# Kernel tuning notes

Measured on AMD Instinct MI355X. Metric: run time of the kernel, lower is better.

## Reference

```python
import jax, jax.numpy as jnp
import numpy as np
import math

S, B, D = 1024, 8, 1024
H = 16
DK = D // H
F = 4096
EPS = 1e-5


def _layernorm(x, g, b):
    m = jnp.mean(x, axis=-1, keepdims=True)
    v = jnp.mean(jnp.square(x - m), axis=-1, keepdims=True)
    return (x - m) * jax.lax.rsqrt(v + EPS) * g + b


def setup_inputs() -> dict:
    key = jax.random.key(0)
    ks = jax.random.split(key, 16)
    sc = 0.02
    inp = {
        "src": jax.random.normal(ks[0], (S, B, D), dtype=jnp.float32),
        "pos": jax.random.normal(ks[1], (S, B, D), dtype=jnp.float32),
        "Wq": jax.random.normal(ks[2], (D, D), dtype=jnp.float32) * sc,
        "bq": jnp.zeros((D,), dtype=jnp.float32),
        "Wk": jax.random.normal(ks[3], (D, D), dtype=jnp.float32) * sc,
        "bk": jnp.zeros((D,), dtype=jnp.float32),
        "Wv": jax.random.normal(ks[4], (D, D), dtype=jnp.float32) * sc,
        "bv": jnp.zeros((D,), dtype=jnp.float32),
        "Wo": jax.random.normal(ks[5], (D, D), dtype=jnp.float32) * sc,
        "bo": jnp.zeros((D,), dtype=jnp.float32),
        "W1": jax.random.normal(ks[6], (D, F), dtype=jnp.float32) * sc,
        "b1": jnp.zeros((F,), dtype=jnp.float32),
        "W2": jax.random.normal(ks[7], (F, D), dtype=jnp.float32) * sc,
        "b2": jnp.zeros((D,), dtype=jnp.float32),
        "g1": jnp.ones((D,), dtype=jnp.float32),
        "be1": jnp.zeros((D,), dtype=jnp.float32),
        "g2": jnp.ones((D,), dtype=jnp.float32),
        "be2": jnp.zeros((D,), dtype=jnp.float32),
    }
    return inp


def reference(src, pos, Wq, bq, Wk, bk, Wv, bv, Wo, bo, W1, b1, W2, b2, g1, be1, g2, be2):
    # post-norm encoder layer; dropout = identity (eval mode)
    qk_in = src + pos                      # q = k = src + pos, value = src
    # to batch-first [B, S, D]
    qb = jnp.transpose(qk_in, (1, 0, 2))
    vb = jnp.transpose(src, (1, 0, 2))

    def split_heads(x):                    # [B,S,D] -> [B,H,S,DK]
        return jnp.transpose(x.reshape(B, S, H, DK), (0, 2, 1, 3))

    q = split_heads(qb @ Wq + bq)
    k = split_heads(qb @ Wk + bk)
    v = split_heads(vb @ Wv + bv)

    scores = jnp.einsum('bhqd,bhkd->bhqk', q, k) / math.sqrt(DK)
    attn = jax.nn.softmax(scores, axis=-1)             # [B,H,S,S]
    ctx = jnp.einsum('bhqk,bhkd->bhqd', attn, v)       # [B,H,S,DK]
    ctx = jnp.transpose(ctx, (0, 2, 1, 3)).reshape(B, S, D)
    attn_out = ctx @ Wo + bo                           # [B,S,D]
    attn_out = jnp.transpose(attn_out, (1, 0, 2))      # back to [S,B,D]

    x = _layernorm(src + attn_out, g1, be1)
    ffn = jax.nn.relu(x @ W1 + b1) @ W2 + b2
    out = _layernorm(x + ffn, g2, be2)
    return out, attn
```

## Files before the change

### kernel.cpp

```cpp
#include <hip/hip_runtime.h>
#include <stdint.h>

#define S_ 1024
#define B_ 8
#define D_ 1024
#define H_ 16
#define DK_ 64
#define F_ 4096
#define EPS_ 1e-5f

typedef __bf16 bf16_t;
typedef __attribute__((ext_vector_type(8))) __bf16 bf16x8;
typedef __attribute__((ext_vector_type(4))) __bf16 bf16x4;
typedef __attribute__((ext_vector_type(4))) float f32x4;

#define GLD16(gp, lp) __builtin_amdgcn_global_load_lds( \
    (__attribute__((address_space(1))) void*)(void*)(gp), \
    (__attribute__((address_space(3))) void*)(lp), 16, 0, 0)

#define BAR() __builtin_amdgcn_s_barrier()
#define SB0() __builtin_amdgcn_sched_barrier(0)
#define LG0() do { asm volatile("s_waitcnt lgkmcnt(0)" ::: "memory"); SB0(); } while (0)
#define VM6() asm volatile("s_waitcnt vmcnt(6)" ::: "memory")

template<int MODE>
__global__ __launch_bounds__(512, 2)
void gemm8p(const bf16_t* __restrict__ A, const bf16_t* __restrict__ Bt,
            const float* __restrict__ bias, const float* __restrict__ bias2,
            void* __restrict__ out, void* __restrict__ out2,
            int K, int lda, int ldb, int ldc)
{
    __shared__ __align__(16) bf16_t AsL[2][256][64];
    __shared__ __align__(16) bf16_t BsL[2][256][64];

    const int nwg = gridDim.x * gridDim.y;
    int flat = blockIdx.y * gridDim.x + blockIdx.x;
    flat = (flat & 7) * (nwg >> 3) + (flat >> 3);
    const int bx = flat % gridDim.x, by = flat / gridDim.x;
    const int rowBase = by * 256, colBase = bx * 256;

    const int tid = threadIdx.x;
    const int lane = tid & 63;
    const int wave = tid >> 6;
    const int wr = wave >> 2, wc = wave & 3;
    const int lr = lane & 15, quad = lane >> 4;

    const int r0 = tid >> 3, r1 = 64 + r0;
    const int cs = (tid & 7) ^ (r0 & 7);
    const int cl = tid & 7;
    const bf16_t* a0p = A + (size_t)(rowBase + r0) * lda + cs * 8;
    const bf16_t* a1p = A + (size_t)(rowBase + r1) * lda + cs * 8;
    const bf16_t* b0p = Bt + (size_t)(colBase + r0) * ldb + cs * 8;
    const bf16_t* b1p = Bt + (size_t)(colBase + r1) * ldb + cs * 8;

#define STAGE_A(buf, h, kel) do { \
    GLD16(a0p + (size_t)(h) * 128 * lda + (kel), &AsL[buf][(h) * 128 + r0][cl * 8]); \
    GLD16(a1p + (size_t)(h) * 128 * lda + (kel), &AsL[buf][(h) * 128 + r1][cl * 8]); } while (0)
#define STAGE_B(buf, h, kel) do { \
    GLD16(b0p + (size_t)(h) * 128 * ldb + (kel), &BsL[buf][(h) * 128 + r0][cl * 8]); \
    GLD16(b1p + (size_t)(h) * 128 * ldb + (kel), &BsL[buf][(h) * 128 + r1][cl * 8]); } while (0)

#define RDA(buf, qm, AF) do { \
    _Pragma("unroll") for (int mi = 0; mi < 4; ++mi) { \
        const int r_ = (qm) * 128 + wr * 64 + mi * 16 + lr; \
        _Pragma("unroll") for (int kk = 0; kk < 2; ++kk) \
            AF[mi * 2 + kk] = *(const bf16x8*)&AsL[buf][r_][((kk * 4 + quad) ^ (lr & 7)) * 8]; } } while (0)
#define RDB(buf, qn, BF) do { \
    _Pragma("unroll") for (int ni = 0; ni < 2; ++ni) { \
        const int r_ = (qn) * 128 + wc * 32 + ni * 16 + lr; \
        _Pragma("unroll") for (int kk = 0; kk < 2; ++kk) \
            BF[ni * 2 + kk] = *(const bf16x8*)&BsL[buf][r_][((kk * 4 + quad) ^ (lr & 7)) * 8]; } } while (0)

#define MQ(qm, qn, AF, BF) do { \
    __builtin_amdgcn_s_setprio(1); \
    _Pragma("unroll") for (int kk = 0; kk < 2; ++kk) \
    _Pragma("unroll") for (int mi = 0; mi < 4; ++mi) \
    _Pragma("unroll") for (int ni = 0; ni < 2; ++ni) \
        acc[(qm) * 4 + mi][(qn) * 2 + ni] = __builtin_amdgcn_mfma_f32_16x16x32_bf16( \
            AF[mi * 2 + kk], BF[ni * 2 + kk], acc[(qm) * 4 + mi][(qn) * 2 + ni], 0, 0, 0); \
    __builtin_amdgcn_s_setprio(0); } while (0)

    f32x4 acc[8][4] = {};
    bf16x8 af[8], bq0[4], bq1[4];

    STAGE_A(0, 0, 0); STAGE_B(0, 0, 0); STAGE_B(0, 1, 0); STAGE_A(0, 1, 0);
    STAGE_A(1, 0, 64); STAGE_B(1, 0, 64); STAGE_B(1, 1, 64);
    VM6();
    BAR(); SB0();

    const int NT = K >> 6;
    const int kCap = K - 64;
    for (int it = 0; it < (NT >> 1); ++it) {
        const int kP1 = it * 128 + 64;
        int kN0 = it * 128 + 128; if (kN0 > kCap) kN0 = kCap;
        int kN1 = it * 128 + 192; if (kN1 > kCap) kN1 = kCap;

        RDA(0, 0, af); RDB(0, 0, bq0);
        STAGE_A(1, 1, kP1);
        BAR(); LG0();
        MQ(0, 0, af, bq0);
        BAR(); SB0();
        RDB(0, 1, bq1);
        STAGE_A(0, 0, kN0);
        BAR(); LG0();
        MQ(0, 1, af, bq1);
        BAR(); SB0();
        RDA(0, 1, af);
        STAGE_B(0, 0, kN0);
        BAR(); LG0();
        MQ(1, 1, af, bq1);
        BAR(); SB0();
        STAGE_B(0, 1, kN0);
        BAR(); SB0();
        MQ(1, 0, af, bq0);
        VM6();
        BAR(); SB0();
        RDA(1, 0, af); RDB(1, 0, bq0);
        STAGE_A(0, 1, kN0);
        BAR(); LG0();
        MQ(0, 0, af, bq0);
        BAR(); SB0();
        RDB(1, 1, bq1);
        STAGE_A(1, 0, kN1);
        BAR(); LG0();
        MQ(0, 1, af, bq1);
        BAR(); SB0();
        RDA(1, 1, af);
        STAGE_B(1, 0, kN1);
        BAR(); LG0();
        MQ(1, 1, af, bq1);
        BAR(); SB0();
        STAGE_B(1, 1, kN1);
        BAR(); SB0();
        MQ(1, 0, af, bq0);
        VM6();
        BAR(); SB0();
    }

#pragma unroll
    for (int mi = 0; mi < 8; ++mi) {
#pragma unroll
        for (int ni = 0; ni < 4; ++ni) {
            const int col = colBase + (ni >> 1) * 128 + wc * 32 + (ni & 1) * 16 + lr;
            float bv;
            if constexpr (MODE == 0) bv = (col < 1024) ? bias[col] : bias2[col - 1024];
            else bv = bias[col];
#pragma unroll
            for (int e = 0; e < 4; ++e) {
                const int row = rowBase + (mi >> 2) * 128 + wr * 64 + (mi & 3) * 16 + quad * 4 + e;
                const float v = acc[mi][ni][e] + bv;
                if constexpr (MODE == 0) {
                    const int sel = col >> 10, c10 = col & 1023;
                    const int s = row >> 3, b = row & 7, h = c10 >> 6, dk = c10 & 63;
                    bf16_t* dst = sel ? (bf16_t*)out2 : (bf16_t*)out;
                    dst[(((size_t)(b * 16 + h) * 1024 + s) << 6) + dk] = (bf16_t)v;
                } else {
                    ((bf16_t*)out)[(size_t)row * ldc + col] = (bf16_t)fmaxf(v, 0.f);
                }
            }
        }
    }
#undef STAGE_A
#undef STAGE_B
#undef RDA
#undef RDB
#undef MQ
}

template<int BM, int BN, int WM, int WN, int MODE>
__global__ __launch_bounds__(256)
void gemm_bt(const bf16_t* __restrict__ A, const bf16_t* __restrict__ Bt,
             const float* __restrict__ bias, void* __restrict__ out,
             int K, int lda, int ldb, int ldc, long batchA, long batchB)
{
    constexpr int MT = WM / 16, NT = WN / 16;
    constexpr int WCOLS = BN / WN;
    __shared__ __align__(16) bf16_t As[BM * 32];
    __shared__ __align__(16) bf16_t Bs[BN * 32];

    const int z = blockIdx.z;
    A += (size_t)z * batchA;
    Bt += (size_t)z * batchB;
    const int rowBase = blockIdx.y * BM;
    const int colBase = blockIdx.x * BN;
    const int tid = threadIdx.x;
    const int wave = tid >> 6, lane = tid & 63;
    const int wr = wave / WCOLS, wc = wave % WCOLS;
    const int lr = lane & 15;
    const int lk = (lane >> 4) * 8;

    f32x4 acc[MT][NT] = {};

    for (int k0 = 0; k0 < K; k0 += 32) {
#pragma unroll
        for (int i = 0; i < BM / 64; ++i) {
            int id = i * 256 + tid;
            GLD16(A + (size_t)(rowBase + (id >> 2)) * lda + k0 + (id & 3) * 8, As + id * 8);
        }
#pragma unroll
        for (int i = 0; i < BN / 64; ++i) {
            int id = i * 256 + tid;
            GLD16(Bt + (size_t)(colBase + (id >> 2)) * ldb + k0 + (id & 3) * 8, Bs + id * 8);
        }
        __syncthreads();
        bf16x8 af[MT], bfr[NT];
#pragma unroll
        for (int mi = 0; mi < MT; ++mi)
            af[mi] = *(const bf16x8*)&As[(wr * WM + mi * 16 + lr) * 32 + lk];
#pragma unroll
        for (int ni = 0; ni < NT; ++ni)
            bfr[ni] = *(const bf16x8*)&Bs[(wc * WN + ni * 16 + lr) * 32 + lk];
#pragma unroll
        for (int mi = 0; mi < MT; ++mi)
#pragma unroll
            for (int ni = 0; ni < NT; ++ni)
                acc[mi][ni] = __builtin_amdgcn_mfma_f32_16x16x32_bf16(af[mi], bfr[ni], acc[mi][ni], 0, 0, 0);
        __syncthreads();
    }

    const int quad = lane >> 4;
#pragma unroll
    for (int mi = 0; mi < MT; ++mi) {
#pragma unroll
        for (int ni = 0; ni < NT; ++ni) {
            const int col = colBase + wc * WN + ni * 16 + lr;
            float bv = bias[col];
#pragma unroll
            for (int e = 0; e < 4; ++e) {
                const int row = rowBase + wr * WM + mi * 16 + quad * 4 + e;
                float v = acc[mi][ni][e] + bv;
                if constexpr (MODE == 0) {
                    ((float*)out)[(size_t)row * ldc + col] = v;
                } else if constexpr (MODE == 2) {
                    int s = row >> 3, b = row & 7, h = col >> 6, dk = col & 63;
                    ((bf16_t*)out)[(((size_t)(b * 16 + h) * 64 + dk) << 10) + s] = (bf16_t)v;
                }
            }
        }
    }
}

__global__ __launch_bounds__(256)
void fused_attn(const bf16_t* __restrict__ qb, const bf16_t* __restrict__ kb,
                const bf16_t* __restrict__ vt, float* __restrict__ attn,
                bf16_t* __restrict__ ctx)
{
    __shared__ __align__(16) bf16_t Psh[32 * 1024];
    __shared__ float smax[4][32];
    __shared__ float ssum[4][32];

    int flat = blockIdx.y * 32 + blockIdx.x;
    flat = (flat & 7) * 512 + (flat >> 3);
    const int z = flat >> 5;
    const int qBase = (flat & 31) * 32;
    const int b = z >> 4, h = z & 15;
    const int tid = threadIdx.x;
    const int wave = tid >> 6, lane = tid & 63;
    const int lr = lane & 15, quad = lane >> 4;

    const bf16_t* Qz = qb + ((size_t)z << 16);
    const bf16_t* Kz = kb + ((size_t)z << 16);
    const bf16_t* Vz = vt + ((size_t)z << 16);
    float* Az = attn + ((size_t)z << 20);

    bf16x8 qf[2][2];
#pragma unroll
    for (int ni = 0; ni < 2; ++ni)
#pragma unroll
        for (int kk = 0; kk < 2; ++kk)
            qf[ni][kk] = *(const bf16x8*)(Qz + (size_t)(qBase + ni * 16 + lr) * 64 + kk * 32 + quad * 8);

    f32x4 acc[16][2] = {};
#pragma unroll
    for (int mi = 0; mi < 16; ++mi) {
        const bf16_t* kp = Kz + (size_t)(wave * 256 + mi * 16 + lr) * 64 + quad * 8;
        bf16x8 kf0 = *(const bf16x8*)kp;
        bf16x8 kf1 = *(const bf16x8*)(kp + 32);
#pragma unroll
        for (int ni = 0; ni < 2; ++ni) {
            acc[mi][ni] = __builtin_amdgcn_mfma_f32_16x16x32_bf16(kf0, qf[ni][0], acc[mi][ni], 0, 0, 0);
            acc[mi][ni] = __builtin_amdgcn_mfma_f32_16x16x32_bf16(kf1, qf[ni][1], acc[mi][ni], 0, 0, 0);
        }
    }

    float mloc[2];
#pragma unroll
    for (int ni = 0; ni < 2; ++ni) {
        float mx = acc[0][ni][0];
#pragma unroll
        for (int mi = 0; mi < 16; ++mi)
            mx = fmaxf(mx, fmaxf(fmaxf(acc[mi][ni][0], acc[mi][ni][1]),
                                 fmaxf(acc[mi][ni][2], acc[mi][ni][3])));
        mx = fmaxf(mx, __shfl_xor(mx, 16, 64));
        mx = fmaxf(mx, __shfl_xor(mx, 32, 64));
        mloc[ni] = mx;
    }
    if (quad == 0) { smax[wave][lr] = mloc[0]; smax[wave][16 + lr] = mloc[1]; }
    __syncthreads();

    float rs[2];
#pragma unroll
    for (int ni = 0; ni < 2; ++ni) {
        const int qh = ni * 16 + lr;
        const float mm = 0.125f * fmaxf(fmaxf(smax[0][qh], smax[1][qh]),
                                        fmaxf(smax[2][qh], smax[3][qh]));
        float s = 0.f;
#pragma unroll
        for (int mi = 0; mi < 16; ++mi)
#pragma unroll
            for (int e = 0; e < 4; ++e) {
                float p = __expf(fmaf(acc[mi][ni][e], 0.125f, -mm));
                acc[mi][ni][e] = p; s += p;
            }
        s += __shfl_xor(s, 16, 64);
        s += __shfl_xor(s, 32, 64);
        rs[ni] = s;
    }
    if (quad == 0) { ssum[wave][lr] = rs[0]; ssum[wave][16 + lr] = rs[1]; }
    __syncthreads();

#pragma unroll
    for (int ni = 0; ni < 2; ++ni) {
        const int qh = ni * 16 + lr;
        const float r = 1.0f / (ssum[0][qh] + ssum[1][qh] + ssum[2][qh] + ssum[3][qh]);
        float* arow = Az + ((size_t)(qBase + qh) << 10);
#pragma unroll
        for (int mi = 0; mi < 16; ++mi) {
            const int k0 = wave * 256 + mi * 16 + quad * 4;
            float4 o;
            o.x = acc[mi][ni][0] * r; o.y = acc[mi][ni][1] * r;
            o.z = acc[mi][ni][2] * r; o.w = acc[mi][ni][3] * r;
            *(float4*)(arow + k0) = o;
            bf16x4 pb;
            pb[0] = (bf16_t)o.x; pb[1] = (bf16_t)o.y; pb[2] = (bf16_t)o.z; pb[3] = (bf16_t)o.w;
            int byte = qh * 2048 + k0 * 2;
            byte ^= (qh & 7) << 4;
            *(bf16x4*)((char*)Psh + byte) = pb;
        }
    }
    __syncthreads();

    f32x4 cacc[2] = {};
#pragma unroll
    for (int kt = 0; kt < 32; ++kt) {
        bf16x8 vf = *(const bf16x8*)(Vz + (size_t)(wave * 16 + lr) * 1024 + kt * 32 + quad * 8);
#pragma unroll
        for (int mi = 0; mi < 2; ++mi) {
            const int qh = mi * 16 + lr;
            int byte = qh * 2048 + (kt * 32 + quad * 8) * 2;
            byte ^= (qh & 7) << 4;
            bf16x8 af = *(const bf16x8*)((const char*)Psh + byte);
            cacc[mi] = __builtin_amdgcn_mfma_f32_16x16x32_bf16(af, vf, cacc[mi], 0, 0, 0);
        }
    }
#pragma unroll
    for (int mi = 0; mi < 2; ++mi)
#pragma unroll
        for (int e = 0; e < 4; ++e) {
            const int s = qBase + mi * 16 + quad * 4 + e;
            ctx[(((size_t)s * 8 + b) << 10) + h * 64 + wave * 16 + lr] = (bf16_t)cacc[mi][e];
        }
}

__global__ __launch_bounds__(256)
void prep_kernel(const float* __restrict__ src, const float* __restrict__ pos,
                 bf16_t* __restrict__ qk, bf16_t* __restrict__ vv)
{
    const size_t i = ((size_t)blockIdx.x * 256 + threadIdx.x) * 4;
    float4 s = *(const float4*)(src + i);
    float4 q = *(const float4*)(pos + i);
    bf16x4 qo, vo;
    qo[0] = (bf16_t)(s.x + q.x); qo[1] = (bf16_t)(s.y + q.y);
    qo[2] = (bf16_t)(s.z + q.z); qo[3] = (bf16_t)(s.w + q.w);
    vo[0] = (bf16_t)s.x; vo[1] = (bf16_t)s.y; vo[2] = (bf16_t)s.z; vo[3] = (bf16_t)s.w;
    *(bf16x4*)(qk + i) = qo;
    *(bf16x4*)(vv + i) = vo;
}

__global__ __launch_bounds__(256)
void transpose_w(const float* __restrict__ W, bf16_t* __restrict__ WT, int K, int N)
{
    __shared__ float t[32][33];
    const int n0 = blockIdx.x * 32, k0 = blockIdx.y * 32;
    const int tx = threadIdx.x & 31;
    const int ty = threadIdx.x >> 5;
#pragma unroll
    for (int j = 0; j < 32; j += 8)
        t[ty + j][tx] = W[(size_t)(k0 + ty + j) * N + n0 + tx];
    __syncthreads();
#pragma unroll
    for (int j = 0; j < 32; j += 8)
        WT[(size_t)(n0 + ty + j) * K + k0 + tx] = (bf16_t)t[tx][ty + j];
}

__global__ __launch_bounds__(256)
void ln_kernel(const float* __restrict__ a, const float* __restrict__ b,
               const float* __restrict__ g, const float* __restrict__ be,
               float* __restrict__ xf, bf16_t* __restrict__ xb, float* __restrict__ outf)
{
    __shared__ float sh[8];
    const int r = blockIdx.x;
    const int t = threadIdx.x;
    float4 va = ((const float4*)(a + ((size_t)r << 10)))[t];
    float4 vb = ((const float4*)(b + ((size_t)r << 10)))[t];
    float x0 = va.x + vb.x, x1 = va.y + vb.y, x2 = va.z + vb.z, x3 = va.w + vb.w;
    float s = x0 + x1 + x2 + x3;
    float sq = x0 * x0 + x1 * x1 + x2 * x2 + x3 * x3;
#pragma unroll
    for (int o = 32; o > 0; o >>= 1) { s += __shfl_xor(s, o, 64); sq += __shfl_xor(sq, o, 64); }
    const int w = t >> 6, ln = t & 63;
    if (ln == 0) { sh[w] = s; sh[4 + w] = sq; }
    __syncthreads();
    s = sh[0] + sh[1] + sh[2] + sh[3];
    sq = sh[4] + sh[5] + sh[6] + sh[7];
    const float mean = s * (1.f / 1024.f);
    const float var = sq * (1.f / 1024.f) - mean * mean;
    const float rstd = rsqrtf(var + EPS_);
    float4 vg = ((const float4*)g)[t];
    float4 vbe = ((const float4*)be)[t];
    float y0 = (x0 - mean) * rstd * vg.x + vbe.x;
    float y1 = (x1 - mean) * rstd * vg.y + vbe.y;
    float y2 = (x2 - mean) * rstd * vg.z + vbe.z;
    float y3 = (x3 - mean) * rstd * vg.w + vbe.w;
    if (xf) { float4 o4 = {y0, y1, y2, y3}; ((float4*)(xf + ((size_t)r << 10)))[t] = o4; }
    if (xb) {
        bf16x4 ob; ob[0] = (bf16_t)y0; ob[1] = (bf16_t)y1; ob[2] = (bf16_t)y2; ob[3] = (bf16_t)y3;
        ((bf16x4*)(xb + ((size_t)r << 10)))[t] = ob;
    }
    if (outf) { float4 o4 = {y0, y1, y2, y3}; ((float4*)(outf + ((size_t)r << 10)))[t] = o4; }
}

extern "C" void kernel_launch(void* const* d_in, const int* in_sizes, int n_in,
                              void* d_out, int out_size, void* d_ws, size_t ws_size,
                              hipStream_t stream)
{
    (void)in_sizes; (void)n_in; (void)out_size; (void)ws_size;
    const float* src = (const float*)d_in[0];
    const float* pos = (const float*)d_in[1];
    const float* Wq  = (const float*)d_in[2];
    const float* bq  = (const float*)d_in[3];
    const float* Wk  = (const float*)d_in[4];
    const float* bk  = (const float*)d_in[5];
    const float* Wv  = (const float*)d_in[6];
    const float* bv  = (const float*)d_in[7];
    const float* Wo  = (const float*)d_in[8];
    const float* bo  = (const float*)d_in[9];
    const float* W1  = (const float*)d_in[10];
    const float* b1  = (const float*)d_in[11];
    const float* W2  = (const float*)d_in[12];
    const float* b2  = (const float*)d_in[13];
    const float* g1  = (const float*)d_in[14];
    const float* be1 = (const float*)d_in[15];
    const float* g2  = (const float*)d_in[16];
    const float* be2 = (const float*)d_in[17];

    float* outF  = (float*)d_out;
    float* attnF = outF + (size_t)S_ * B_ * D_;

    char* ws = (char*)d_ws;
    size_t off = 0;
    auto alloc = [&](size_t bytes) { void* p = ws + off; off += (bytes + 255) & ~(size_t)255; return p; };

    bf16_t* qk_bf = (bf16_t*)alloc((size_t)8192 * 1024 * 2);
    bf16_t* v_bf  = (bf16_t*)alloc((size_t)8192 * 1024 * 2);
    bf16_t* wqT   = (bf16_t*)alloc((size_t)1024 * 1024 * 2);
    bf16_t* wkT   = (bf16_t*)alloc((size_t)1024 * 1024 * 2);
    bf16_t* wvT   = (bf16_t*)alloc((size_t)1024 * 1024 * 2);
    bf16_t* woT   = (bf16_t*)alloc((size_t)1024 * 1024 * 2);
    bf16_t* w1T   = (bf16_t*)alloc((size_t)4096 * 1024 * 2);
    bf16_t* w2T   = (bf16_t*)alloc((size_t)1024 * 4096 * 2);
    bf16_t* qbuf  = (bf16_t*)alloc((size_t)8 * 16 * 1024 * 64 * 2);
    bf16_t* kbuf  = (bf16_t*)alloc((size_t)8 * 16 * 1024 * 64 * 2);
    bf16_t* vtbuf = (bf16_t*)alloc((size_t)8 * 16 * 64 * 1024 * 2);
    bf16_t* ctx_bf= (bf16_t*)alloc((size_t)8192 * 1024 * 2);
    float*  ao_f  = (float*)alloc((size_t)8192 * 1024 * 4);
    float*  x_f   = (float*)alloc((size_t)8192 * 1024 * 4);
    bf16_t* x_bf  = (bf16_t*)alloc((size_t)8192 * 1024 * 2);
    bf16_t* h_bf  = (bf16_t*)alloc((size_t)8192 * 4096 * 2);
    float*  y_f   = (float*)alloc((size_t)8192 * 1024 * 4);

    transpose_w<<<dim3(32, 32), 256, 0, stream>>>(Wq, wqT, 1024, 1024);
    transpose_w<<<dim3(32, 32), 256, 0, stream>>>(Wk, wkT, 1024, 1024);
    transpose_w<<<dim3(32, 32), 256, 0, stream>>>(Wv, wvT, 1024, 1024);
    transpose_w<<<dim3(32, 32), 256, 0, stream>>>(Wo, woT, 1024, 1024);
    transpose_w<<<dim3(128, 32), 256, 0, stream>>>(W1, w1T, 1024, 4096);
    transpose_w<<<dim3(32, 128), 256, 0, stream>>>(W2, w2T, 4096, 1024);

    prep_kernel<<<8192, 256, 0, stream>>>(src, pos, qk_bf, v_bf);

    gemm8p<0><<<dim3(8, 32), 512, 0, stream>>>(qk_bf, wqT, bq, bk, qbuf, kbuf, 1024, 1024, 1024, 0);
    gemm_bt<128, 128, 64, 64, 2><<<dim3(8, 64, 1), 256, 0, stream>>>(v_bf, wvT, bv, vtbuf, 1024, 1024, 1024, 0, 0, 0);

    fused_attn<<<dim3(32, 128), 256, 0, stream>>>(qbuf, kbuf, vtbuf, attnF, ctx_bf);

    gemm_bt<128, 128, 64, 64, 0><<<dim3(8, 64, 1), 256, 0, stream>>>(ctx_bf, woT, bo, ao_f, 1024, 1024, 1024, 1024, 0, 0);

    ln_kernel<<<8192, 256, 0, stream>>>(src, ao_f, g1, be1, x_f, x_bf, nullptr);

    gemm8p<1><<<dim3(16, 32), 512, 0, stream>>>(x_bf, w1T, b1, nullptr, h_bf, nullptr, 1024, 1024, 1024, 4096);
    gemm_bt<128, 128, 64, 64, 0><<<dim3(8, 64, 1), 256, 0, stream>>>(h_bf, w2T, b2, y_f, 4096, 4096, 4096, 1024, 0, 0);

    ln_kernel<<<8192, 256, 0, stream>>>(x_f, y_f, g2, be2, nullptr, nullptr, outF);
}
```

Measured before the change: 654.4 us.

## Replace simple GEMMs with pipelined 256x128 swizzled-LDS kernel and batch weight transposes

Replaces the single-buffered 128x128 gemm_bt with a new gemm4p kernel for the V, output and FFN2 projections. gemm4p uses 256x128 tiles with 512 threads, double-buffered LDS with XOR swizzling, and async global-to-LDS staging interleaved with MFMA phases under s_setprio. This is meant to hide global load latency and cut LDS bank conflicts in these GEMMs. The four DxD weight transposes are also merged into one launch. The cost is higher register and LDS pressure, and a more fragile hand-tuned wait and barrier schedule.

```diff
diff --git a/kernel.cpp b/kernel.cpp
--- a/kernel.cpp
+++ b/kernel.cpp
@@ -22,6 +22,8 @@
 #define SB0() __builtin_amdgcn_sched_barrier(0)
 #define LG0() do { asm volatile("s_waitcnt lgkmcnt(0)" ::: "memory"); SB0(); } while (0)
 #define VM6() asm volatile("s_waitcnt vmcnt(6)" ::: "memory")
+#define VM4() asm volatile("s_waitcnt vmcnt(4)" ::: "memory")
+#define VM3() asm volatile("s_waitcnt vmcnt(3)" ::: "memory")
 
 template<int MODE>
 __global__ __launch_bounds__(512, 2)
@@ -167,77 +169,123 @@
 #undef MQ
 }
 
-template<int BM, int BN, int WM, int WN, int MODE>
-__global__ __launch_bounds__(256)
-void gemm_bt(const bf16_t* __restrict__ A, const bf16_t* __restrict__ Bt,
-             const float* __restrict__ bias, void* __restrict__ out,
-             int K, int lda, int ldb, int ldc, long batchA, long batchB)
-{
-    constexpr int MT = WM / 16, NT = WN / 16;
-    constexpr int WCOLS = BN / WN;
-    __shared__ __align__(16) bf16_t As[BM * 32];
-    __shared__ __align__(16) bf16_t Bs[BN * 32];
-
-    const int z = blockIdx.z;
-    A += (size_t)z * batchA;
-    Bt += (size_t)z * batchB;
-    const int rowBase = blockIdx.y * BM;
-    const int colBase = blockIdx.x * BN;
+template<int MODE>
+__global__ __launch_bounds__(512, 2)
+void gemm4p(const bf16_t* __restrict__ A, const bf16_t* __restrict__ Bt,
+            const float* __restrict__ bias, void* __restrict__ out,
+            int K, int lda, int ldb, int ldc)
+{
+    __shared__ __align__(16) bf16_t AsL[2][256][64];
+    __shared__ __align__(16) bf16_t BsL[2][128][64];
+
+    const int nwg = gridDim.x * gridDim.y;
+    int flat = blockIdx.y * gridDim.x + blockIdx.x;
+    flat = (flat & 7) * (nwg >> 3) + (flat >> 3);
+    const int bx = flat % gridDim.x, by = flat / gridDim.x;
+    const int rowBase = by * 256, colBase = bx * 128;
+
     const int tid = threadIdx.x;
-    const int wave = tid >> 6, lane = tid & 63;
-    const int wr = wave / WCOLS, wc = wave % WCOLS;
-    const int lr = lane & 15;
-    const int lk = (lane >> 4) * 8;
-
-    f32x4 acc[MT][NT] = {};
-
-    for (int k0 = 0; k0 < K; k0 += 32) {
-#pragma unroll
-        for (int i = 0; i < BM / 64; ++i) {
-            int id = i * 256 + tid;
-            GLD16(A + (size_t)(rowBase + (id >> 2)) * lda + k0 + (id & 3) * 8, As + id * 8);
-        }
-#pragma unroll
-        for (int i = 0; i < BN / 64; ++i) {
-            int id = i * 256 + tid;
-            GLD16(Bt + (size_t)(colBase + (id >> 2)) * ldb + k0 + (id & 3) * 8, Bs + id * 8);
-        }
-        __syncthreads();
-        bf16x8 af[MT], bfr[NT];
-#pragma unroll
-        for (int mi = 0; mi < MT; ++mi)
-            af[mi] = *(const bf16x8*)&As[(wr * WM + mi * 16 + lr) * 32 + lk];
-#pragma unroll
-        for (int ni = 0; ni < NT; ++ni)
-            bfr[ni] = *(const bf16x8*)&Bs[(wc * WN + ni * 16 + lr) * 32 + lk];
-#pragma unroll
-        for (int mi = 0; mi < MT; ++mi)
-#pragma unroll
-            for (int ni = 0; ni < NT; ++ni)
-                acc[mi][ni] = __builtin_amdgcn_mfma_f32_16x16x32_bf16(af[mi], bfr[ni], acc[mi][ni], 0, 0, 0);
-        __syncthreads();
-    }
-
-    const int quad = lane >> 4;
-#pragma unroll
-    for (int mi = 0; mi < MT; ++mi) {
-#pragma unroll
-        for (int ni = 0; ni < NT; ++ni) {
-            const int col = colBase + wc * WN + ni * 16 + lr;
-            float bv = bias[col];
+    const int lane = tid & 63;
+    const int wave = tid >> 6;
+    const int wr = wave >> 2, wc = wave & 3;
+    const int lr = lane & 15, quad = lane >> 4;
+
+    const int r0 = tid >> 3, r1 = 64 + r0;
+    const int cs = (tid & 7) ^ (r0 & 7);
+    const int cl = tid & 7;
+    const bf16_t* a0p = A + (size_t)(rowBase + r0) * lda + cs * 8;
+    const bf16_t* a1p = A + (size_t)(rowBase + r1) * lda + cs * 8;
+    const bf16_t* b0p = Bt + (size_t)(colBase + r0) * ldb + cs * 8;
+
+#define STAGE_A(buf, h, kel) do { \
+    GLD16(a0p + (size_t)(h) * 128 * lda + (kel), &AsL[buf][(h) * 128 + r0][cl * 8]); \
+    GLD16(a1p + (size_t)(h) * 128 * lda + (kel), &AsL[buf][(h) * 128 + r1][cl * 8]); } while (0)
+#define STAGE_B(buf, h, kel) \
+    GLD16(b0p + (size_t)(h) * 64 * ldb + (kel), &BsL[buf][(h) * 64 + r0][cl * 8])
+
+#define RDA(buf, qm, AF) do { \
+    _Pragma("unroll") for (int mi = 0; mi < 4; ++mi) { \
+        const int r_ = (qm) * 128 + wr * 64 + mi * 16 + lr; \
+        _Pragma("unroll") for (int kk = 0; kk < 2; ++kk) \
+            AF[mi * 2 + kk] = *(const bf16x8*)&AsL[buf][r_][((kk * 4 + quad) ^ (lr & 7)) * 8]; } } while (0)
+#define RDBF(buf, BQ) do { \
+    _Pragma("unroll") for (int qn = 0; qn < 2; ++qn) { \
+        const int r_ = qn * 64 + wc * 16 + lr; \
+        _Pragma("unroll") for (int kk = 0; kk < 2; ++kk) \
+            BQ[qn * 2 + kk] = *(const bf16x8*)&BsL[buf][r_][((kk * 4 + quad) ^ (lr & 7)) * 8]; } } while (0)
+
+#define MQA(qm) do { \
+    __builtin_amdgcn_s_setprio(1); \
+    _Pragma("unroll") for (int kk = 0; kk < 2; ++kk) \
+    _Pragma("unroll") for (int mi = 0; mi < 4; ++mi) \
+    _Pragma("unroll") for (int qn = 0; qn < 2; ++qn) \
+        acc[(qm) * 4 + mi][qn] = __builtin_amdgcn_mfma_f32_16x16x32_bf16( \
+            af[mi * 2 + kk], bq[qn * 2 + kk], acc[(qm) * 4 + mi][qn], 0, 0, 0); \
+    __builtin_amdgcn_s_setprio(0); } while (0)
+
+    f32x4 acc[8][2] = {};
+    bf16x8 af[8], bq[4];
+
+    STAGE_A(0, 0, 0); STAGE_B(0, 0, 0); STAGE_B(0, 1, 0); STAGE_A(0, 1, 0);
+    STAGE_A(1, 0, 64); STAGE_B(1, 0, 64); STAGE_B(1, 1, 64);
+    VM4();
+    BAR(); SB0();
+
+    const int NT = K >> 6;
+    const int kCap = K - 64;
+    for (int it = 0; it < (NT >> 1); ++it) {
+        const int kP1 = it * 128 + 64;
+        int kN0 = it * 128 + 128; if (kN0 > kCap) kN0 = kCap;
+        int kN1 = it * 128 + 192; if (kN1 > kCap) kN1 = kCap;
+
+        RDA(0, 0, af); RDBF(0, bq);
+        STAGE_A(1, 1, kP1);
+        BAR(); LG0();
+        MQA(0);
+        BAR(); SB0();
+        RDA(0, 1, af);
+        STAGE_A(0, 0, kN0); STAGE_B(0, 0, kN0);
+        BAR(); LG0();
+        MQA(1);
+        VM3();
+        BAR(); SB0();
+        RDA(1, 0, af); RDBF(1, bq);
+        STAGE_B(0, 1, kN0); STAGE_A(0, 1, kN0);
+        BAR(); LG0();
+        MQA(0);
+        BAR(); SB0();
+        RDA(1, 1, af);
+        STAGE_A(1, 0, kN1); STAGE_B(1, 0, kN1); STAGE_B(1, 1, kN1);
+        BAR(); LG0();
+        MQA(1);
+        VM4();
+        BAR(); SB0();
+    }
+
+#pragma unroll
+    for (int mi = 0; mi < 8; ++mi) {
+#pragma unroll
+        for (int ni = 0; ni < 2; ++ni) {
+            const int col = colBase + ni * 64 + wc * 16 + lr;
+            const float bv = bias[col];
 #pragma unroll
             for (int e = 0; e < 4; ++e) {
-                const int row = rowBase + wr * WM + mi * 16 + quad * 4 + e;
-                float v = acc[mi][ni][e] + bv;
+                const int row = rowBase + (mi >> 2) * 128 + wr * 64 + (mi & 3) * 16 + quad * 4 + e;
+                const float v = acc[mi][ni][e] + bv;
                 if constexpr (MODE == 0) {
                     ((float*)out)[(size_t)row * ldc + col] = v;
-                } else if constexpr (MODE == 2) {
-                    int s = row >> 3, b = row & 7, h = col >> 6, dk = col & 63;
+                } else {
+                    const int s = row >> 3, b = row & 7, h = col >> 6, dk = col & 63;
                     ((bf16_t*)out)[(((size_t)(b * 16 + h) * 64 + dk) << 10) + s] = (bf16_t)v;
                 }
             }
         }
     }
+#undef STAGE_A
+#undef STAGE_B
+#undef RDA
+#undef RDBF
+#undef MQA
 }
 
 __global__ __launch_bounds__(256)
@@ -375,6 +423,32 @@
     vo[0] = (bf16_t)s.x; vo[1] = (bf16_t)s.y; vo[2] = (bf16_t)s.z; vo[3] = (bf16_t)s.w;
     *(bf16x4*)(qk + i) = qo;
     *(bf16x4*)(vv + i) = vo;
+}
+
+__global__ __launch_bounds__(256)
+void transpose_w4(const float* __restrict__ W0, const float* __restrict__ W1,
+                  const float* __restrict__ W2, const float* __restrict__ W3,
+                  bf16_t* __restrict__ T0, bf16_t* __restrict__ T1,
+                  bf16_t* __restrict__ T2, bf16_t* __restrict__ T3)
+{
+    __shared__ float t[32][33];
+    const float* W; bf16_t* T;
+    switch (blockIdx.z) {
+        case 0: W = W0; T = T0; break;
+        case 1: W = W1; T = T1; break;
+        case 2: W = W2; T = T2; break;
+        default: W = W3; T = T3; break;
+    }
+    const int n0 = blockIdx.x * 32, k0 = blockIdx.y * 32;
+    const int tx = threadIdx.x & 31;
+    const int ty = threadIdx.x >> 5;
+#pragma unroll
+    for (int j = 0; j < 32; j += 8)
+        t[ty + j][tx] = W[(size_t)(k0 + ty + j) * 1024 + n0 + tx];
+    __syncthreads();
+#pragma unroll
+    for (int j = 0; j < 32; j += 8)
+        T[(size_t)(n0 + ty + j) * 1024 + k0 + tx] = (bf16_t)t[tx][ty + j];
 }
 
 __global__ __launch_bounds__(256)
@@ -479,26 +553,23 @@
     bf16_t* h_bf  = (bf16_t*)alloc((size_t)8192 * 4096 * 2);
     float*  y_f   = (float*)alloc((size_t)8192 * 1024 * 4);
 
-    transpose_w<<<dim3(32, 32), 256, 0, stream>>>(Wq, wqT, 1024, 1024);
-    transpose_w<<<dim3(32, 32), 256, 0, stream>>>(Wk, wkT, 1024, 1024);
-    transpose_w<<<dim3(32, 32), 256, 0, stream>>>(Wv, wvT, 1024, 1024);
-    transpose_w<<<dim3(32, 32), 256, 0, stream>>>(Wo, woT, 1024, 1024);
+    transpose_w4<<<dim3(32, 32, 4), 256, 0, stream>>>(Wq, Wk, Wv, Wo, wqT, wkT, wvT, woT);
     transpose_w<<<dim3(128, 32), 256, 0, stream>>>(W1, w1T, 1024, 4096);
     transpose_w<<<dim3(32, 128), 256, 0, stream>>>(W2, w2T, 4096, 1024);
 
     prep_kernel<<<8192, 256, 0, stream>>>(src, pos, qk_bf, v_bf);
 
     gemm8p<0><<<dim3(8, 32), 512, 0, stream>>>(qk_bf, wqT, bq, bk, qbuf, kbuf, 1024, 1024, 1024, 0);
-    gemm_bt<128, 128, 64, 64, 2><<<dim3(8, 64, 1), 256, 0, stream>>>(v_bf, wvT, bv, vtbuf, 1024, 1024, 1024, 0, 0, 0);
+    gemm4p<2><<<dim3(8, 32), 512, 0, stream>>>(v_bf, wvT, bv, vtbuf, 1024, 1024, 1024, 0);
 
     fused_attn<<<dim3(32, 128), 256, 0, stream>>>(qbuf, kbuf, vtbuf, attnF, ctx_bf);
 
-    gemm_bt<128, 128, 64, 64, 0><<<dim3(8, 64, 1), 256, 0, stream>>>(ctx_bf, woT, bo, ao_f, 1024, 1024, 1024, 1024, 0, 0);
+    gemm4p<0><<<dim3(8, 32), 512, 0, stream>>>(ctx_bf, woT, bo, ao_f, 1024, 1024, 1024, 1024);
 
     ln_kernel<<<8192, 256, 0, stream>>>(src, ao_f, g1, be1, x_f, x_bf, nullptr);
 
     gemm8p<1><<<dim3(16, 32), 512, 0, stream>>>(x_bf, w1T, b1, nullptr, h_bf, nullptr, 1024, 1024, 1024, 4096);
-    gemm_bt<128, 128, 64, 64, 0><<<dim3(8, 64, 1), 256, 0, stream>>>(h_bf, w2T, b2, y_f, 4096, 4096, 4096, 1024, 0, 0);
+    gemm4p<0><<<dim3(8, 32), 512, 0, stream>>>(h_bf, w2T, b2, y_f, 4096, 4096, 4096, 1024);
 
     ln_kernel<<<8192, 256, 0, stream>>>(x_f, y_f, g2, be2, nullptr, nullptr, outF);
 }
```

After: 592.3 us. 9.5% less time.
